# Performance work log

Hardware: AMD Instinct MI355X
Metric: run time of the kernel (lower is better)

The kernel has to match this reference:

```python
import jax, jax.numpy as jnp
import numpy as np
from jax import lax

NUM_HEADS = 8
HEAD_SIZE = 256  # hidden_size // num_heads

def _layernorm(x, g, b, eps=1e-5):
    mu = jnp.mean(x, axis=-1, keepdims=True)
    var = jnp.mean((x - mu) ** 2, axis=-1, keepdims=True)
    return (x - mu) * lax.rsqrt(var + eps) * g + b

def _groupnorm(x, g, b, num_groups, eps=1e-5):
    B, C = x.shape
    xr = x.reshape(B, num_groups, C // num_groups)
    mu = jnp.mean(xr, axis=-1, keepdims=True)
    var = jnp.mean((xr - mu) ** 2, axis=-1, keepdims=True)
    xn = ((xr - mu) * lax.rsqrt(var + eps)).reshape(B, C)
    return xn * g + b

def _block_diag(x, W, b):
    # x: (B, nb*fi), W: (nb, fi, fo), b: (nb, fo) -> (B, nb*fo)
    B = x.shape[0]
    nb, fi, fo = W.shape
    y = jnp.einsum('bnf,nfo->bno', x.reshape(B, nb, fi), W) + b
    return y.reshape(B, nb * fo)

def _causal_conv1d(x, w, b):
    # x: (B, L); w: (1,1,4). Pad-both-sides-3 then drop last 3 == left-pad 3.
    y = lax.conv_general_dilated(x[:, None, :], w, (1,), [(3, 0)])
    return y[:, 0, :] + b

def _mlstm_forward(x, ln_g, ln_b, Wupl, bupl, Wupr, bupr, conv_w, conv_b,
                   Wskip, bskip, Wq, bq, Wk, bk, Wv, bv, Wi, bi, Wf, bf,
                   Wo, bo, gn_g, gn_b, Wdown, bdown, c_prev, n_prev, m_prev):
    x_norm = _layernorm(x, ln_g, ln_b)
    x_up_left = x_norm @ Wupl + bupl           # (B, 2D)
    x_up_right = x_norm @ Wupr + bupr          # (B, H)
    x_conv = jax.nn.silu(_causal_conv1d(x_up_left, conv_w, conv_b))
    x_skip = x_conv @ Wskip + bskip            # (B, H)
    q = _block_diag(x_conv, Wq, bq)
    k = _block_diag(x_conv, Wk, bk) / (HEAD_SIZE ** 0.5)
    v = _block_diag(x_up_left, Wv, bv)
    i_tilde = x_conv @ Wi + bi
    f_tilde = x_conv @ Wf + bf
    o = jax.nn.sigmoid(x_up_left @ Wo + bo)
    m_t = jnp.maximum(f_tilde + m_prev, i_tilde)
    i_g = jnp.exp(i_tilde - m_t)
    f_g = jnp.exp(f_tilde + m_prev - m_t)
    c_t = f_g * c_prev + i_g * (v * k)
    n_t = f_g * n_prev + i_g * k
    denom = jnp.max(jnp.abs(n_t.T @ q), axis=1)  # (H,) broadcast over batch
    h_t = o * (c_t * q) / denom
    out = _groupnorm(h_t, gn_g, gn_b, NUM_HEADS) + x_skip
    out = out * jax.nn.silu(x_up_right)
    final = out @ Wdown + bdown + x
    return (final, h_t, c_t, n_t, m_t)

def setup_inputs():
    key = jax.random.key(0)
    ks = jax.random.split(key, 16)
    B, D, H, NB = 8192, 1024, 2048, 8
    UP = 2 * D
    rnd = lambda k, shp, s=0.02: jax.random.normal(k, shp, jnp.float32) * s
    return {
        'x': jax.random.normal(ks[0], (B, D), jnp.float32),
        'ln_g': jnp.ones((D,), jnp.float32), 'ln_b': jnp.zeros((D,), jnp.float32),
        'Wupl': rnd(ks[1], (D, UP)), 'bupl': jnp.zeros((UP,), jnp.float32),
        'Wupr': rnd(ks[2], (D, H)), 'bupr': jnp.zeros((H,), jnp.float32),
        'conv_w': rnd(ks[3], (1, 1, 4), 0.3), 'conv_b': jnp.zeros((1,), jnp.float32),
        'Wskip': rnd(ks[4], (UP, H)), 'bskip': jnp.zeros((H,), jnp.float32),
        'Wq': rnd(ks[5], (NB, UP // NB, H // NB)), 'bq': jnp.zeros((NB, H // NB), jnp.float32),
        'Wk': rnd(ks[6], (NB, UP // NB, H // NB)), 'bk': jnp.zeros((NB, H // NB), jnp.float32),
        'Wv': rnd(ks[7], (NB, UP // NB, H // NB)), 'bv': jnp.zeros((NB, H // NB), jnp.float32),
        'Wi': rnd(ks[8], (UP, H)), 'bi': jnp.zeros((H,), jnp.float32),
        'Wf': rnd(ks[9], (UP, H)), 'bf': jnp.zeros((H,), jnp.float32),
        'Wo': rnd(ks[10], (UP, H)), 'bo': jnp.zeros((H,), jnp.float32),
        'gn_g': jnp.ones((H,), jnp.float32), 'gn_b': jnp.zeros((H,), jnp.float32),
        'Wdown': rnd(ks[11], (H, D)), 'bdown': jnp.zeros((D,), jnp.float32),
        'c_prev': rnd(ks[12], (B, H)), 'n_prev': jnp.ones((B, H), jnp.float32),
        'm_prev': jnp.zeros((B, H), jnp.float32),
    }

def reference(x, ln_g, ln_b, Wupl, bupl, Wupr, bupr, conv_w, conv_b, Wskip, bskip,
              Wq, bq, Wk, bk, Wv, bv, Wi, bi, Wf, bf, Wo, bo, gn_g, gn_b,
              Wdown, bdown, c_prev, n_prev, m_prev):
    return _mlstm_forward(x, ln_g, ln_b, Wupl, bupl, Wupr, bupr, conv_w, conv_b,
                          Wskip, bskip, Wq, bq, Wk, bk, Wv, bv, Wi, bi, Wf, bf,
                          Wo, bo, gn_g, gn_b, Wdown, bdown, c_prev, n_prev, m_prev)
```

## Files before the change

### kernel.cpp

```cpp
#include <hip/hip_runtime.h>


typedef __bf16 bf16_t;
typedef bf16_t bf16x8 __attribute__((ext_vector_type(8)));
typedef bf16_t bf16x4 __attribute__((ext_vector_type(4)));
typedef float f32x4 __attribute__((ext_vector_type(4)));

#define B_ROWS 8192
#define DMODEL 1024
#define HDIM   2048

__device__ __forceinline__ void gload_lds16(const void* g, void* s) {
  __builtin_amdgcn_global_load_lds(
      (const __attribute__((address_space(1))) void*)g,
      (__attribute__((address_space(3))) void*)s, 16, 0, 0);
}

__device__ __forceinline__ float sigmoidf_(float x) { return 1.f / (1.f + __expf(-x)); }
__device__ __forceinline__ float siluf_(float x)    { return x / (1.f + __expf(-x)); }

__device__ __forceinline__ int xcd_swz(int lin, int nwg) {
  const int q = nwg >> 3, r = nwg & 7;
  const int xcd = lin & 7, sub = lin >> 3;
  return (xcd < r ? xcd * (q + 1) : r * (q + 1) + (xcd - r) * q) + sub;
}

__global__ __launch_bounds__(256) void wtrans_kernel(
    const float* __restrict__ in, bf16_t* __restrict__ out, int R, int C) {
  const int z = blockIdx.z;
  in  += (size_t)z * R * C;
  out += (size_t)z * R * C;
  __shared__ float tile[64][65];
  const int t = threadIdx.x;
  const int r0 = blockIdx.y * 64, c0 = blockIdx.x * 64;
#pragma unroll
  for (int j = 0; j < 4; ++j) {
    const int r = j * 16 + (t >> 4);
    const int c = (t & 15) * 4;
    float4 v = *(const float4*)&in[(size_t)(r0 + r) * C + c0 + c];
    tile[r][c] = v.x; tile[r][c + 1] = v.y; tile[r][c + 2] = v.z; tile[r][c + 3] = v.w;
  }
  __syncthreads();
#pragma unroll
  for (int j = 0; j < 2; ++j) {
    const int wi = j * 256 + t;
    const int oc = wi >> 3;
    const int orr = (wi & 7) * 8;
    bf16x8 v;
#pragma unroll
    for (int u = 0; u < 8; ++u) v[u] = (bf16_t)tile[orr + u][oc];
    *(bf16x8*)&out[(size_t)(c0 + oc) * R + r0 + orr] = v;
  }
}

__global__ __launch_bounds__(256) void ln_kernel(
    const float* __restrict__ x, const float* __restrict__ g,
    const float* __restrict__ b, bf16_t* __restrict__ out) {
  const int row = blockIdx.x;
  const int t = threadIdx.x;
  const float* xr = x + (size_t)row * DMODEL;
  float4 v = *(const float4*)&xr[t * 4];
  float s = v.x + v.y + v.z + v.w;
  float s2 = v.x * v.x + v.y * v.y + v.z * v.z + v.w * v.w;
#pragma unroll
  for (int off = 1; off < 64; off <<= 1) {
    s += __shfl_xor(s, off, 64);
    s2 += __shfl_xor(s2, off, 64);
  }
  __shared__ float ps[8];
  const int w = t >> 6;
  if ((t & 63) == 0) { ps[w] = s; ps[4 + w] = s2; }
  __syncthreads();
  s = ps[0] + ps[1] + ps[2] + ps[3];
  s2 = ps[4] + ps[5] + ps[6] + ps[7];
  const float mu = s / (float)DMODEL;
  const float var = s2 / (float)DMODEL - mu * mu;
  const float rstd = rsqrtf(var + 1e-5f);
  float4 gg = *(const float4*)&g[t * 4];
  float4 bb = *(const float4*)&b[t * 4];
  bf16x4 o;
  o[0] = (bf16_t)((v.x - mu) * rstd * gg.x + bb.x);
  o[1] = (bf16_t)((v.y - mu) * rstd * gg.y + bb.y);
  o[2] = (bf16_t)((v.z - mu) * rstd * gg.z + bb.z);
  o[3] = (bf16_t)((v.w - mu) * rstd * gg.w + bb.w);
  *(bf16x4*)&out[(size_t)row * DMODEL + t * 4] = o;
}

__global__ __launch_bounds__(256) void conv_kernel(
    const bf16_t* __restrict__ xin, const float* __restrict__ cw,
    const float* __restrict__ cb, bf16_t* __restrict__ yb) {
  const size_t idx = (size_t)blockIdx.x * blockDim.x + threadIdx.x;
  const int row = (int)(idx >> 9);
  const int c0 = ((int)idx & 511) * 4;
  const bf16_t* xr = xin + (size_t)row * HDIM;
  const float w0 = cw[0], w1 = cw[1], w2 = cw[2], w3 = cw[3], bb = cb[0];
  float xm3 = 0.f, xm2 = 0.f, xm1 = 0.f;
  if (c0 > 0) {
    bf16x4 p = *(const bf16x4*)&xr[c0 - 4];
    xm3 = (float)p[1]; xm2 = (float)p[2]; xm1 = (float)p[3];
  }
  bf16x4 xv4 = *(const bf16x4*)&xr[c0];
  float x0 = (float)xv4[0], x1 = (float)xv4[1], x2 = (float)xv4[2], x3 = (float)xv4[3];
  float y0 = w0 * xm3 + w1 * xm2 + w2 * xm1 + w3 * x0 + bb;
  float y1 = w0 * xm2 + w1 * xm1 + w2 * x0 + w3 * x1 + bb;
  float y2 = w0 * xm1 + w1 * x0 + w2 * x1 + w3 * x2 + bb;
  float y3 = w0 * x0 + w1 * x1 + w2 * x2 + w3 * x3 + bb;
  bf16x4 yb4;
  yb4[0] = (bf16_t)siluf_(y0); yb4[1] = (bf16_t)siluf_(y1);
  yb4[2] = (bf16_t)siluf_(y2); yb4[3] = (bf16_t)siluf_(y3);
  *(bf16x4*)&yb[(size_t)row * HDIM + c0] = yb4;
}

__global__ __launch_bounds__(256) void hgn_kernel(
    const bf16_t* __restrict__ o_pre, const float* __restrict__ q,
    const float* __restrict__ c_t, const float* __restrict__ denomf,
    const bf16_t* __restrict__ skip, const bf16_t* __restrict__ upr,
    const float* __restrict__ gn_g, const float* __restrict__ gn_b,
    float* __restrict__ h_out, bf16_t* __restrict__ act_out) {
  const int row = blockIdx.x;
  const int t = threadIdx.x;
  const size_t base = (size_t)row * HDIM + t * 8;
  const int i0 = t * 8;
  bf16x8 o8 = *(const bf16x8*)&o_pre[base];
  float h[8];
  float s = 0.f, s2 = 0.f;
#pragma unroll
  for (int j = 0; j < 2; ++j) {
    float4 qv = *(const float4*)&q[base + j * 4];
    float4 cv = *(const float4*)&c_t[base + j * 4];
#pragma unroll
    for (int u = 0; u < 4; ++u) {
      const int k = j * 4 + u;
      float hv = sigmoidf_((float)o8[k]) * ((const float*)&cv)[u] *
                 ((const float*)&qv)[u] / denomf[i0 + k];
      h[k] = hv;
      s += hv;
      s2 += hv * hv;
    }
  }
#pragma unroll
  for (int off = 1; off < 32; off <<= 1) {
    s += __shfl_xor(s, off, 64);
    s2 += __shfl_xor(s2, off, 64);
  }
  const float mu = s / 256.f;
  const float var = s2 / 256.f - mu * mu;
  const float rstd = rsqrtf(var + 1e-5f);
  float4 h0 = {h[0], h[1], h[2], h[3]};
  float4 h1 = {h[4], h[5], h[6], h[7]};
  *(float4*)&h_out[base] = h0;
  *(float4*)&h_out[base + 4] = h1;
  bf16x8 sk8 = *(const bf16x8*)&skip[base];
  bf16x8 up8 = *(const bf16x8*)&upr[base];
  bf16x8 a8;
#pragma unroll
  for (int j = 0; j < 2; ++j) {
    float4 gv = *(const float4*)&gn_g[i0 + j * 4];
    float4 bv = *(const float4*)&gn_b[i0 + j * 4];
#pragma unroll
    for (int u = 0; u < 4; ++u) {
      const int k = j * 4 + u;
      float y = (h[k] - mu) * rstd * ((const float*)&gv)[u] + ((const float*)&bv)[u];
      y = (y + (float)sk8[k]) * siluf_((float)up8[k]);
      a8[k] = (bf16_t)y;
    }
  }
  *(bf16x8*)&act_out[base] = a8;
}

template <int OUTMODE, bool RES>
__global__ __launch_bounds__(256) void gemm_kernel(
    const bf16_t* __restrict__ A, int lda, const bf16_t* __restrict__ Bt, int ldb,
    const float* __restrict__ bias, float* __restrict__ C, bf16_t* __restrict__ Cb,
    int ldc, const float* __restrict__ res, int ldres, int K, float scale,
    int zA, long long zB, int zBias, int zC) {
  const int z = blockIdx.z;
  A += (size_t)z * zA;
  Bt += (size_t)z * zB;
  if (bias) bias += (size_t)z * zBias;
  if (OUTMODE == 0) C += (size_t)z * zC; else Cb += (size_t)z * zC;
  const int brow = blockIdx.y * 128;
  const int bcol = blockIdx.x * 128;
  __shared__ bf16_t As[128 * 32];
  __shared__ bf16_t Bs[128 * 32];
  const int tid = threadIdx.x;
  const int w = tid >> 6, l = tid & 63;
  const int wr = w >> 1, wc = w & 1;
  const int lr = l & 15, kg = l >> 4;
  const int l4 = l & 3, ld4 = l >> 2;

  f32x4 acc[4][4];
  const f32x4 fzero = {0.f, 0.f, 0.f, 0.f};
#pragma unroll
  for (int m = 0; m < 4; ++m)
#pragma unroll
    for (int n = 0; n < 4; ++n) acc[m][n] = fzero;

  for (int kt = 0; kt < K; kt += 32) {
#pragma unroll
    for (int j = 0; j < 2; ++j) {
      const int rowX = w * 32 + j * 16 + ld4;
      gload_lds16(A + (size_t)(brow + rowX) * lda + kt + l4 * 8, &As[w * 1024 + j * 512]);
      gload_lds16(Bt + (size_t)(bcol + rowX) * ldb + kt + l4 * 8, &Bs[w * 1024 + j * 512]);
    }
    __syncthreads();
    bf16x8 a[4], b[4];
#pragma unroll
    for (int m = 0; m < 4; ++m)
      a[m] = *(const bf16x8*)&As[(wr * 64 + m * 16 + lr) * 32 + kg * 8];
#pragma unroll
    for (int n = 0; n < 4; ++n)
      b[n] = *(const bf16x8*)&Bs[(wc * 64 + n * 16 + lr) * 32 + kg * 8];
#pragma unroll
    for (int m = 0; m < 4; ++m)
#pragma unroll
      for (int n = 0; n < 4; ++n)
        acc[m][n] = __builtin_amdgcn_mfma_f32_16x16x32_bf16(a[m], b[n], acc[m][n], 0, 0, 0);
    __syncthreads();
  }

#pragma unroll
  for (int m = 0; m < 4; ++m) {
    const int row0 = brow + wr * 64 + m * 16 + kg * 4;
#pragma unroll
    for (int n = 0; n < 4; ++n) {
      const int col = bcol + wc * 64 + n * 16 + lr;
      const float bv = bias ? bias[col] : 0.f;
#pragma unroll
      for (int r = 0; r < 4; ++r) {
        const int row = row0 + r;
        float v = (acc[m][n][r] + bv) * scale;
        if (RES) v += res[(size_t)row * ldres + col];
        if (OUTMODE == 0) C[(size_t)row * ldc + col] = v;
        else Cb[(size_t)row * ldc + col] = (bf16_t)v;
      }
    }
  }
}

template <int OUTMODE , bool RES>
__global__ __launch_bounds__(512, 2) void gemm256_kernel(
    const bf16_t* __restrict__ A, int lda, const bf16_t* __restrict__ Bt, int ldb,
    const float* __restrict__ bias, float* __restrict__ C, bf16_t* __restrict__ Cb,
    int ldc, const float* __restrict__ res, int ldres, int K, float scale,
    long long zA, long long zB, long long zC) {
  const int z = blockIdx.z;
  A += (size_t)z * zA;
  Bt += (size_t)z * zB;
  if (OUTMODE == 0) C += (size_t)z * zC; else Cb += (size_t)z * zC;

  const int nwg = gridDim.x * gridDim.y;
  const int lin2 = xcd_swz(blockIdx.y * gridDim.x + blockIdx.x, nwg);
  const int bx = lin2 % gridDim.x, by = lin2 / gridDim.x;
  const int brow = by * 256, bcol = bx * 256;

  __shared__ bf16_t As[2][256 * 64];
  __shared__ bf16_t Bs[2][256 * 64];

  const int tid = threadIdx.x;
  const int l = tid & 63;
  const int w = tid >> 6;
  const int wr = w >> 2, wn = w & 3;
  const int lr = l & 15, kg = l >> 4;
  const int srow = tid >> 3;
  const int sslot = (tid & 7) ^ (srow & 7);

  f32x4 acc[8][4];
  const f32x4 fzero = {0.f, 0.f, 0.f, 0.f};
#pragma unroll
  for (int m = 0; m < 8; ++m)
#pragma unroll
    for (int n = 0; n < 4; ++n) acc[m][n] = fzero;

  const int NT = K >> 6;
  const bf16_t* Ag = A + (size_t)brow * lda;
  const bf16_t* Bg = Bt + (size_t)bcol * ldb;

  auto stage = [&](int t, int buf) {
    const size_t kof = (size_t)t * 64 + sslot * 8;
#pragma unroll
    for (int j = 0; j < 4; ++j) {
      const int r = j * 64 + srow;
      gload_lds16(Ag + (size_t)r * lda + kof, (char*)&As[buf][0] + (j * 512 + tid) * 16);
      gload_lds16(Bg + (size_t)r * ldb + kof, (char*)&Bs[buf][0] + (j * 512 + tid) * 16);
    }
  };

  stage(0, 0);
  stage(1, 1);

  for (int t = 0; t < NT; ++t) {
    if (t < NT - 1) asm volatile("s_waitcnt vmcnt(8)" ::: "memory");
    else            asm volatile("s_waitcnt vmcnt(0)" ::: "memory");
    __builtin_amdgcn_s_barrier();
    const int buf = t & 1;
#pragma unroll
    for (int kk = 0; kk < 2; ++kk) {
      bf16x8 a[8], b[4];
#pragma unroll
      for (int n = 0; n < 4; ++n) {
        const int r = wn * 64 + n * 16 + lr;
        b[n] = *(const bf16x8*)&Bs[buf][r * 64 + (((kk * 4 + kg) ^ (r & 7)) * 8)];
      }
#pragma unroll
      for (int m = 0; m < 8; ++m) {
        const int r = wr * 128 + m * 16 + lr;
        a[m] = *(const bf16x8*)&As[buf][r * 64 + (((kk * 4 + kg) ^ (r & 7)) * 8)];
      }
      __builtin_amdgcn_s_setprio(1);
#pragma unroll
      for (int m = 0; m < 8; ++m)
#pragma unroll
        for (int n = 0; n < 4; ++n)
          acc[m][n] = __builtin_amdgcn_mfma_f32_16x16x32_bf16(a[m], b[n], acc[m][n], 0, 0, 0);
      __builtin_amdgcn_s_setprio(0);
    }
    asm volatile("s_waitcnt lgkmcnt(0)" ::: "memory");
    __builtin_amdgcn_sched_barrier(0);
    __builtin_amdgcn_s_barrier();
    if (t + 2 < NT) stage(t + 2, buf);
  }

#pragma unroll
  for (int m = 0; m < 8; ++m) {
    const int row0 = brow + wr * 128 + m * 16 + kg * 4;
#pragma unroll
    for (int n = 0; n < 4; ++n) {
      const int col = bcol + wn * 64 + n * 16 + lr;
      const float bvv = bias ? bias[col] : 0.f;
#pragma unroll
      for (int r = 0; r < 4; ++r) {
        const int row = row0 + r;
        float v = (acc[m][n][r] + bvv) * scale;
        if (RES) v += res[(size_t)row * ldres + col];
        if (OUTMODE == 0) C[(size_t)row * ldc + col] = v;
        else Cb[(size_t)row * ldc + col] = (bf16_t)v;
      }
    }
  }
}

__global__ __launch_bounds__(512, 2) void ifgate256_kernel(
    const bf16_t* __restrict__ A,
    const bf16_t* __restrict__ Bi, const bf16_t* __restrict__ Bf,
    const float* __restrict__ bi, const float* __restrict__ bfv,
    const float* __restrict__ m_prev, const float* __restrict__ c_prev,
    const float* __restrict__ n_prev,
    const bf16_t* __restrict__ vb, const bf16_t* __restrict__ kb,
    float* __restrict__ m_out, float* __restrict__ c_out, float* __restrict__ n_out) {
  const int nwg = gridDim.x * gridDim.y;
  const int lin2 = xcd_swz(blockIdx.y * gridDim.x + blockIdx.x, nwg);
  const int bx = lin2 % gridDim.x, by = lin2 / gridDim.x;
  const int brow = by * 256, bcol = bx * 128;

  __shared__ bf16_t As[2][256 * 64];
  __shared__ bf16_t Bis[2][128 * 64];
  __shared__ bf16_t Bfs[2][128 * 64];

  const int tid = threadIdx.x;
  const int l = tid & 63;
  const int w = tid >> 6;
  const int wr = w >> 2, wn = w & 3;
  const int lr = l & 15, kg = l >> 4;
  const int srow = tid >> 3;
  const int sslot = (tid & 7) ^ (srow & 7);

  f32x4 acci[8][2], accf[8][2];
  const f32x4 fzero = {0.f, 0.f, 0.f, 0.f};
#pragma unroll
  for (int m = 0; m < 8; ++m)
#pragma unroll
    for (int n = 0; n < 2; ++n) { acci[m][n] = fzero; accf[m][n] = fzero; }

  const int NT = HDIM >> 6;
  const bf16_t* Ag = A + (size_t)brow * HDIM;
  const bf16_t* Big = Bi + (size_t)bcol * HDIM;
  const bf16_t* Bfg = Bf + (size_t)bcol * HDIM;

  auto stage = [&](int t, int buf) {
    const size_t kof = (size_t)t * 64 + sslot * 8;
#pragma unroll
    for (int j = 0; j < 4; ++j) {
      const int r = j * 64 + srow;
      gload_lds16(Ag + (size_t)r * HDIM + kof, (char*)&As[buf][0] + (j * 512 + tid) * 16);
    }
#pragma unroll
    for (int j = 0; j < 2; ++j) {
      const int r = j * 64 + srow;
      gload_lds16(Big + (size_t)r * HDIM + kof, (char*)&Bis[buf][0] + (j * 512 + tid) * 16);
      gload_lds16(Bfg + (size_t)r * HDIM + kof, (char*)&Bfs[buf][0] + (j * 512 + tid) * 16);
    }
  };

  stage(0, 0);
  stage(1, 1);

  for (int t = 0; t < NT; ++t) {
    if (t < NT - 1) asm volatile("s_waitcnt vmcnt(8)" ::: "memory");
    else            asm volatile("s_waitcnt vmcnt(0)" ::: "memory");
    __builtin_amdgcn_s_barrier();
    const int buf = t & 1;
#pragma unroll
    for (int kk = 0; kk < 2; ++kk) {
      bf16x8 a[8], b1[2], b2[2];
#pragma unroll
      for (int n = 0; n < 2; ++n) {
        const int r = wn * 32 + n * 16 + lr;
        const int eo = r * 64 + (((kk * 4 + kg) ^ (r & 7)) * 8);
        b1[n] = *(const bf16x8*)&Bis[buf][eo];
        b2[n] = *(const bf16x8*)&Bfs[buf][eo];
      }
#pragma unroll
      for (int m = 0; m < 8; ++m) {
        const int r = wr * 128 + m * 16 + lr;
        a[m] = *(const bf16x8*)&As[buf][r * 64 + (((kk * 4 + kg) ^ (r & 7)) * 8)];
      }
      __builtin_amdgcn_s_setprio(1);
#pragma unroll
      for (int m = 0; m < 8; ++m)
#pragma unroll
        for (int n = 0; n < 2; ++n) {
          acci[m][n] = __builtin_amdgcn_mfma_f32_16x16x32_bf16(a[m], b1[n], acci[m][n], 0, 0, 0);
          accf[m][n] = __builtin_amdgcn_mfma_f32_16x16x32_bf16(a[m], b2[n], accf[m][n], 0, 0, 0);
        }
      __builtin_amdgcn_s_setprio(0);
    }
    asm volatile("s_waitcnt lgkmcnt(0)" ::: "memory");
    __builtin_amdgcn_sched_barrier(0);
    __builtin_amdgcn_s_barrier();
    if (t + 2 < NT) stage(t + 2, buf);
  }

#pragma unroll
  for (int m = 0; m < 8; ++m) {
    const int row0 = brow + wr * 128 + m * 16 + kg * 4;
#pragma unroll
    for (int n = 0; n < 2; ++n) {
      const int col = bcol + wn * 32 + n * 16 + lr;
      const float biv = bi[col], bfvv = bfv[col];
#pragma unroll
      for (int r = 0; r < 4; ++r) {
        const int row = row0 + r;
        const size_t idx = (size_t)row * HDIM + col;
        const float it = acci[m][n][r] + biv;
        const float ft = accf[m][n][r] + bfvv;
        const float m1 = m_prev[idx];
        const float mt = fmaxf(ft + m1, it);
        const float ig = __expf(it - mt);
        const float fg = __expf(ft + m1 - mt);
        const float v1 = (float)vb[idx], k1 = (float)kb[idx];
        m_out[idx] = mt;
        c_out[idx] = fg * c_prev[idx] + ig * (v1 * k1);
        n_out[idx] = fg * n_prev[idx] + ig * k1;
      }
    }
  }
}

__global__ __launch_bounds__(256) void denom_reduce_kernel(
    const float* __restrict__ part, float* __restrict__ dmaxf) {
  const int i = blockIdx.x;
  const int t = threadIdx.x;
  float vmax = 0.f;
#pragma unroll
  for (int u = 0; u < 8; ++u) {
    const int j = u * 256 + t;
    float s = 0.f;
#pragma unroll
    for (int zz = 0; zz < 4; ++zz)
      s += part[(size_t)zz * HDIM * HDIM + (size_t)i * HDIM + j];
    vmax = fmaxf(vmax, fabsf(s));
  }
#pragma unroll
  for (int off = 1; off < 64; off <<= 1) vmax = fmaxf(vmax, __shfl_xor(vmax, off, 64));
  __shared__ float ps[4];
  if ((t & 63) == 0) ps[t >> 6] = vmax;
  __syncthreads();
  if (t == 0) dmaxf[i] = fmaxf(fmaxf(ps[0], ps[1]), fmaxf(ps[2], ps[3]));
}

extern "C" void kernel_launch(void* const* d_in, const int* in_sizes, int n_in,
                              void* d_out, int out_size, void* d_ws, size_t ws_size,
                              hipStream_t stream) {
  (void)in_sizes; (void)n_in; (void)out_size; (void)ws_size;
  const float* x      = (const float*)d_in[0];
  const float* ln_g   = (const float*)d_in[1];
  const float* ln_b   = (const float*)d_in[2];
  const float* Wupl   = (const float*)d_in[3];
  const float* bupl   = (const float*)d_in[4];
  const float* Wupr   = (const float*)d_in[5];
  const float* bupr   = (const float*)d_in[6];
  const float* conv_w = (const float*)d_in[7];
  const float* conv_b = (const float*)d_in[8];
  const float* Wskip  = (const float*)d_in[9];
  const float* bskip  = (const float*)d_in[10];
  const float* Wq     = (const float*)d_in[11];
  const float* bq     = (const float*)d_in[12];
  const float* Wk     = (const float*)d_in[13];
  const float* bk     = (const float*)d_in[14];
  const float* Wv     = (const float*)d_in[15];
  const float* bv     = (const float*)d_in[16];
  const float* Wi     = (const float*)d_in[17];
  const float* bi     = (const float*)d_in[18];
  const float* Wf     = (const float*)d_in[19];
  const float* bf_    = (const float*)d_in[20];
  const float* Wo     = (const float*)d_in[21];
  const float* bo     = (const float*)d_in[22];
  const float* gn_g   = (const float*)d_in[23];
  const float* gn_b   = (const float*)d_in[24];
  const float* Wdown  = (const float*)d_in[25];
  const float* bdown  = (const float*)d_in[26];
  const float* c_prev = (const float*)d_in[27];
  const float* n_prev = (const float*)d_in[28];
  const float* m_prev = (const float*)d_in[29];

  float* out_final = (float*)d_out;
  float* out_h = out_final + (size_t)B_ROWS * DMODEL;
  float* out_c = out_h + (size_t)B_ROWS * HDIM;
  float* out_n = out_c + (size_t)B_ROWS * HDIM;
  float* out_m = out_n + (size_t)B_ROWS * HDIM;

  char* ws = (char*)d_ws;
  size_t off = 0;
  auto alloc = [&](size_t bytes) -> void* {
    off = (off + 255) & ~(size_t)255;
    void* p = ws + off;
    off += bytes;
    return p;
  };
  const size_t BH = (size_t)B_ROWS * HDIM;
  const size_t BD = (size_t)B_ROWS * DMODEL;

  bf16_t* WuplT = (bf16_t*)alloc((size_t)DMODEL * HDIM * 2);
  bf16_t* WuprT = (bf16_t*)alloc((size_t)DMODEL * HDIM * 2);
  bf16_t* WskipT = (bf16_t*)alloc((size_t)HDIM * HDIM * 2);
  bf16_t* WiT = (bf16_t*)alloc((size_t)HDIM * HDIM * 2);
  bf16_t* WfT = (bf16_t*)alloc((size_t)HDIM * HDIM * 2);
  bf16_t* WoT = (bf16_t*)alloc((size_t)HDIM * HDIM * 2);
  bf16_t* WdownT = (bf16_t*)alloc((size_t)HDIM * DMODEL * 2);
  bf16_t* WqT = (bf16_t*)alloc((size_t)8 * 256 * 256 * 2);
  bf16_t* WkT = (bf16_t*)alloc((size_t)8 * 256 * 256 * 2);
  bf16_t* WvT = (bf16_t*)alloc((size_t)8 * 256 * 256 * 2);
  bf16_t* xnorm_b = (bf16_t*)alloc(BD * 2);
  bf16_t* xupl_b = (bf16_t*)alloc(BH * 2);
  bf16_t* xupr_b = (bf16_t*)alloc(BH * 2);
  bf16_t* xconv_b = (bf16_t*)alloc(BH * 2);
  bf16_t* xskip_b = (bf16_t*)alloc(BH * 2);
  bf16_t* o_b = (bf16_t*)alloc(BH * 2);
  float*  q_f = (float*)alloc(BH * 4);
  bf16_t* k_b = (bf16_t*)alloc(BH * 2);
  bf16_t* v_b = (bf16_t*)alloc(BH * 2);
  bf16_t* qT_b = (bf16_t*)alloc(BH * 2);
  bf16_t* nT_b = (bf16_t*)alloc(BH * 2);
  bf16_t* act_b = (bf16_t*)alloc(BH * 2);
  float*  part = (float*)alloc((size_t)4 * HDIM * HDIM * 4);
  float*  dmaxf = (float*)alloc(HDIM * 4);

  wtrans_kernel<<<dim3(HDIM / 64, DMODEL / 64, 1), 256, 0, stream>>>(Wupl, WuplT, DMODEL, HDIM);
  wtrans_kernel<<<dim3(HDIM / 64, DMODEL / 64, 1), 256, 0, stream>>>(Wupr, WuprT, DMODEL, HDIM);
  wtrans_kernel<<<dim3(HDIM / 64, HDIM / 64, 1), 256, 0, stream>>>(Wskip, WskipT, HDIM, HDIM);
  wtrans_kernel<<<dim3(HDIM / 64, HDIM / 64, 1), 256, 0, stream>>>(Wi, WiT, HDIM, HDIM);
  wtrans_kernel<<<dim3(HDIM / 64, HDIM / 64, 1), 256, 0, stream>>>(Wf, WfT, HDIM, HDIM);
  wtrans_kernel<<<dim3(HDIM / 64, HDIM / 64, 1), 256, 0, stream>>>(Wo, WoT, HDIM, HDIM);
  wtrans_kernel<<<dim3(DMODEL / 64, HDIM / 64, 1), 256, 0, stream>>>(Wdown, WdownT, HDIM, DMODEL);
  wtrans_kernel<<<dim3(4, 4, 8), 256, 0, stream>>>(Wq, WqT, 256, 256);
  wtrans_kernel<<<dim3(4, 4, 8), 256, 0, stream>>>(Wk, WkT, 256, 256);
  wtrans_kernel<<<dim3(4, 4, 8), 256, 0, stream>>>(Wv, WvT, 256, 256);

  ln_kernel<<<B_ROWS, 256, 0, stream>>>(x, ln_g, ln_b, xnorm_b);

  gemm256_kernel<2, false><<<dim3(HDIM / 256, B_ROWS / 256, 1), 512, 0, stream>>>(
      xnorm_b, DMODEL, WuplT, DMODEL, bupl, nullptr, xupl_b, HDIM, nullptr, 0,
      DMODEL, 1.f, 0, 0, 0);
  gemm256_kernel<2, false><<<dim3(HDIM / 256, B_ROWS / 256, 1), 512, 0, stream>>>(
      xnorm_b, DMODEL, WuprT, DMODEL, bupr, nullptr, xupr_b, HDIM, nullptr, 0,
      DMODEL, 1.f, 0, 0, 0);

  conv_kernel<<<(unsigned)(BH / 4 / 256), 256, 0, stream>>>(xupl_b, conv_w, conv_b, xconv_b);

  gemm256_kernel<2, false><<<dim3(HDIM / 256, B_ROWS / 256, 1), 512, 0, stream>>>(
      xconv_b, HDIM, WskipT, HDIM, bskip, nullptr, xskip_b, HDIM, nullptr, 0,
      HDIM, 1.f, 0, 0, 0);
  gemm256_kernel<2, false><<<dim3(HDIM / 256, B_ROWS / 256, 1), 512, 0, stream>>>(
      xupl_b, HDIM, WoT, HDIM, bo, nullptr, o_b, HDIM, nullptr, 0,
      HDIM, 1.f, 0, 0, 0);

  gemm_kernel<0, false><<<dim3(2, B_ROWS / 128, 8), 256, 0, stream>>>(
      xconv_b, HDIM, WqT, 256, bq, q_f, nullptr, HDIM, nullptr, 0,
      256, 1.f, 256, 256 * 256, 256, 256);
  gemm_kernel<2, false><<<dim3(2, B_ROWS / 128, 8), 256, 0, stream>>>(
      xconv_b, HDIM, WkT, 256, bk, nullptr, k_b, HDIM, nullptr, 0,
      256, 0.0625f, 256, 256 * 256, 256, 256);
  gemm_kernel<2, false><<<dim3(2, B_ROWS / 128, 8), 256, 0, stream>>>(
      xupl_b, HDIM, WvT, 256, bv, nullptr, v_b, HDIM, nullptr, 0,
      256, 1.f, 256, 256 * 256, 256, 256);

  ifgate256_kernel<<<dim3(HDIM / 128, B_ROWS / 256, 1), 512, 0, stream>>>(
      xconv_b, WiT, WfT, bi, bf_, m_prev, c_prev, n_prev, v_b, k_b,
      out_m, out_c, out_n);

  wtrans_kernel<<<dim3(HDIM / 64, B_ROWS / 64, 1), 256, 0, stream>>>(q_f, qT_b, B_ROWS, HDIM);
  wtrans_kernel<<<dim3(HDIM / 64, B_ROWS / 64, 1), 256, 0, stream>>>(out_n, nT_b, B_ROWS, HDIM);

  gemm256_kernel<0, false><<<dim3(HDIM / 256, HDIM / 256, 4), 512, 0, stream>>>(
      nT_b, B_ROWS, qT_b, B_ROWS, nullptr, part, nullptr, HDIM, nullptr, 0,
      2048, 1.f, 2048, 2048, (long long)HDIM * HDIM);
  denom_reduce_kernel<<<HDIM, 256, 0, stream>>>(part, dmaxf);

  hgn_kernel<<<B_ROWS, 256, 0, stream>>>(o_b, q_f, out_c, dmaxf, xskip_b,
                                         xupr_b, gn_g, gn_b, out_h, act_b);

  gemm256_kernel<0, true><<<dim3(DMODEL / 256, B_ROWS / 256, 1), 512, 0, stream>>>(
      act_b, HDIM, WdownT, HDIM, bdown, out_final, nullptr, DMODEL, x, DMODEL,
      HDIM, 1.f, 0, 0, 0);
}
```

Measured before the change: 1.351 ms.

## Split GEMM K-tiles into half-stages with finer-grained prefetch; store q in bf16

The main GEMM kernels now split each 64-wide K tile into two 32-wide halves with a new swizzle. Loads for the next tile are issued in between MFMA groups, with per-half waitcnt and barrier, so global-to-LDS traffic overlaps compute more finely and the trailing lgkmcnt wait and barrier go away. The q projection is stored as bf16 instead of fp32, which halves its write and read traffic and needs a new bf16 transpose kernel. The down projection uses a new 256x128-tile GEMM to put more workgroups on the N=1024 output. Risks are extra barriers per tile and slightly lower precision for q in h_t.

```diff
diff --git a/kernel.cpp b/kernel.cpp
--- a/kernel.cpp
+++ b/kernel.cpp
@@ -39,6 +39,32 @@
     const int c = (t & 15) * 4;
     float4 v = *(const float4*)&in[(size_t)(r0 + r) * C + c0 + c];
     tile[r][c] = v.x; tile[r][c + 1] = v.y; tile[r][c + 2] = v.z; tile[r][c + 3] = v.w;
+  }
+  __syncthreads();
+#pragma unroll
+  for (int j = 0; j < 2; ++j) {
+    const int wi = j * 256 + t;
+    const int oc = wi >> 3;
+    const int orr = (wi & 7) * 8;
+    bf16x8 v;
+#pragma unroll
+    for (int u = 0; u < 8; ++u) v[u] = (bf16_t)tile[orr + u][oc];
+    *(bf16x8*)&out[(size_t)(c0 + oc) * R + r0 + orr] = v;
+  }
+}
+
+__global__ __launch_bounds__(256) void wtransb_kernel(
+    const bf16_t* __restrict__ in, bf16_t* __restrict__ out, int R, int C) {
+  __shared__ float tile[64][65];
+  const int t = threadIdx.x;
+  const int r0 = blockIdx.y * 64, c0 = blockIdx.x * 64;
+#pragma unroll
+  for (int j = 0; j < 4; ++j) {
+    const int r = j * 16 + (t >> 4);
+    const int c = (t & 15) * 4;
+    bf16x4 v = *(const bf16x4*)&in[(size_t)(r0 + r) * C + c0 + c];
+    tile[r][c] = (float)v[0]; tile[r][c + 1] = (float)v[1];
+    tile[r][c + 2] = (float)v[2]; tile[r][c + 3] = (float)v[3];
   }
   __syncthreads();
 #pragma unroll
@@ -112,7 +138,7 @@
 }
 
 __global__ __launch_bounds__(256) void hgn_kernel(
-    const bf16_t* __restrict__ o_pre, const float* __restrict__ q,
+    const bf16_t* __restrict__ o_pre, const bf16_t* __restrict__ q,
     const float* __restrict__ c_t, const float* __restrict__ denomf,
     const bf16_t* __restrict__ skip, const bf16_t* __restrict__ upr,
     const float* __restrict__ gn_g, const float* __restrict__ gn_b,
@@ -122,17 +148,17 @@
   const size_t base = (size_t)row * HDIM + t * 8;
   const int i0 = t * 8;
   bf16x8 o8 = *(const bf16x8*)&o_pre[base];
+  bf16x8 q8 = *(const bf16x8*)&q[base];
   float h[8];
   float s = 0.f, s2 = 0.f;
 #pragma unroll
   for (int j = 0; j < 2; ++j) {
-    float4 qv = *(const float4*)&q[base + j * 4];
     float4 cv = *(const float4*)&c_t[base + j * 4];
 #pragma unroll
     for (int u = 0; u < 4; ++u) {
       const int k = j * 4 + u;
       float hv = sigmoidf_((float)o8[k]) * ((const float*)&cv)[u] *
-                 ((const float*)&qv)[u] / denomf[i0 + k];
+                 (float)q8[k] / denomf[i0 + k];
       h[k] = hv;
       s += hv;
       s2 += hv * hv;
@@ -238,6 +264,8 @@
   }
 }
 
+#define SWZ_RD(r, kg) (((kg) ^ (((r) >> 1) & 3)) * 8)
+
 template <int OUTMODE , bool RES>
 __global__ __launch_bounds__(512, 2) void gemm256_kernel(
     const bf16_t* __restrict__ A, int lda, const bf16_t* __restrict__ Bt, int ldb,
@@ -254,16 +282,14 @@
   const int bx = lin2 % gridDim.x, by = lin2 / gridDim.x;
   const int brow = by * 256, bcol = bx * 256;
 
-  __shared__ bf16_t As[2][256 * 64];
-  __shared__ bf16_t Bs[2][256 * 64];
+  __shared__ bf16_t As[2][2][256 * 32];
+  __shared__ bf16_t Bs[2][2][256 * 32];
 
   const int tid = threadIdx.x;
   const int l = tid & 63;
   const int w = tid >> 6;
   const int wr = w >> 2, wn = w & 3;
   const int lr = l & 15, kg = l >> 4;
-  const int srow = tid >> 3;
-  const int sslot = (tid & 7) ^ (srow & 7);
 
   f32x4 acc[8][4];
   const f32x4 fzero = {0.f, 0.f, 0.f, 0.f};
@@ -276,49 +302,103 @@
   const bf16_t* Ag = A + (size_t)brow * lda;
   const bf16_t* Bg = Bt + (size_t)bcol * ldb;
 
-  auto stage = [&](int t, int buf) {
-    const size_t kof = (size_t)t * 64 + sslot * 8;
-#pragma unroll
-    for (int j = 0; j < 4; ++j) {
-      const int r = j * 64 + srow;
-      gload_lds16(Ag + (size_t)r * lda + kof, (char*)&As[buf][0] + (j * 512 + tid) * 16);
-      gload_lds16(Bg + (size_t)r * ldb + kof, (char*)&Bs[buf][0] + (j * 512 + tid) * 16);
+  auto stageA = [&](int d, int kh, int kbase) {
+#pragma unroll
+    for (int j = 0; j < 2; ++j) {
+      const int L = j * 512 + tid;
+      const int row = L >> 2;
+      const int s = (L & 3) ^ ((L >> 3) & 3);
+      gload_lds16(Ag + (size_t)row * lda + kbase + kh * 32 + s * 8,
+                  (char*)&As[d][kh][0] + L * 16);
     }
   };
-
-  stage(0, 0);
-  stage(1, 1);
+  auto stageB = [&](int d, int kh, int kbase) {
+#pragma unroll
+    for (int j = 0; j < 2; ++j) {
+      const int L = j * 512 + tid;
+      const int row = L >> 2;
+      const int s = (L & 3) ^ ((L >> 3) & 3);
+      gload_lds16(Bg + (size_t)row * ldb + kbase + kh * 32 + s * 8,
+                  (char*)&Bs[d][kh][0] + L * 16);
+    }
+  };
+
+  stageA(0, 0, 0); stageB(0, 0, 0); stageA(0, 1, 0); stageB(0, 1, 0);
 
   for (int t = 0; t < NT; ++t) {
-    if (t < NT - 1) asm volatile("s_waitcnt vmcnt(8)" ::: "memory");
-    else            asm volatile("s_waitcnt vmcnt(0)" ::: "memory");
+    const int d = t & 1;
+    const int kn = (t + 1) * 64;
+    const bool st = (t + 1 < NT);
+    bf16x8 a[4], b[4];
+
+    asm volatile("s_waitcnt vmcnt(4)" ::: "memory");
     __builtin_amdgcn_s_barrier();
-    const int buf = t & 1;
-#pragma unroll
-    for (int kk = 0; kk < 2; ++kk) {
-      bf16x8 a[8], b[4];
-#pragma unroll
-      for (int n = 0; n < 4; ++n) {
-        const int r = wn * 64 + n * 16 + lr;
-        b[n] = *(const bf16x8*)&Bs[buf][r * 64 + (((kk * 4 + kg) ^ (r & 7)) * 8)];
-      }
-#pragma unroll
-      for (int m = 0; m < 8; ++m) {
-        const int r = wr * 128 + m * 16 + lr;
-        a[m] = *(const bf16x8*)&As[buf][r * 64 + (((kk * 4 + kg) ^ (r & 7)) * 8)];
-      }
-      __builtin_amdgcn_s_setprio(1);
-#pragma unroll
-      for (int m = 0; m < 8; ++m)
-#pragma unroll
-        for (int n = 0; n < 4; ++n)
-          acc[m][n] = __builtin_amdgcn_mfma_f32_16x16x32_bf16(a[m], b[n], acc[m][n], 0, 0, 0);
-      __builtin_amdgcn_s_setprio(0);
-    }
-    asm volatile("s_waitcnt lgkmcnt(0)" ::: "memory");
-    __builtin_amdgcn_sched_barrier(0);
+    if (st) stageA(d ^ 1, 0, kn);
+#pragma unroll
+    for (int n = 0; n < 4; ++n) {
+      const int r = wn * 64 + n * 16 + lr;
+      b[n] = *(const bf16x8*)&Bs[d][0][r * 32 + SWZ_RD(r, kg)];
+    }
+#pragma unroll
+    for (int mm = 0; mm < 4; ++mm) {
+      const int r = wr * 128 + mm * 16 + lr;
+      a[mm] = *(const bf16x8*)&As[d][0][r * 32 + SWZ_RD(r, kg)];
+    }
+    __builtin_amdgcn_s_setprio(1);
+#pragma unroll
+    for (int mm = 0; mm < 4; ++mm)
+#pragma unroll
+      for (int n = 0; n < 4; ++n)
+        acc[mm][n] = __builtin_amdgcn_mfma_f32_16x16x32_bf16(a[mm], b[n], acc[mm][n], 0, 0, 0);
+    __builtin_amdgcn_s_setprio(0);
+    if (st) stageB(d ^ 1, 0, kn);
+#pragma unroll
+    for (int mm = 0; mm < 4; ++mm) {
+      const int r = wr * 128 + (4 + mm) * 16 + lr;
+      a[mm] = *(const bf16x8*)&As[d][0][r * 32 + SWZ_RD(r, kg)];
+    }
+    __builtin_amdgcn_s_setprio(1);
+#pragma unroll
+    for (int mm = 0; mm < 4; ++mm)
+#pragma unroll
+      for (int n = 0; n < 4; ++n)
+        acc[4 + mm][n] = __builtin_amdgcn_mfma_f32_16x16x32_bf16(a[mm], b[n], acc[4 + mm][n], 0, 0, 0);
+    __builtin_amdgcn_s_setprio(0);
+
+    if (t == NT - 1) asm volatile("s_waitcnt vmcnt(0)" ::: "memory");
+    else             asm volatile("s_waitcnt vmcnt(4)" ::: "memory");
     __builtin_amdgcn_s_barrier();
-    if (t + 2 < NT) stage(t + 2, buf);
+    if (st) stageA(d ^ 1, 1, kn);
+#pragma unroll
+    for (int n = 0; n < 4; ++n) {
+      const int r = wn * 64 + n * 16 + lr;
+      b[n] = *(const bf16x8*)&Bs[d][1][r * 32 + SWZ_RD(r, kg)];
+    }
+#pragma unroll
+    for (int mm = 0; mm < 4; ++mm) {
+      const int r = wr * 128 + mm * 16 + lr;
+      a[mm] = *(const bf16x8*)&As[d][1][r * 32 + SWZ_RD(r, kg)];
+    }
+    __builtin_amdgcn_s_setprio(1);
+#pragma unroll
+    for (int mm = 0; mm < 4; ++mm)
+#pragma unroll
+      for (int n = 0; n < 4; ++n)
+        acc[mm][n] = __builtin_amdgcn_mfma_f32_16x16x32_bf16(a[mm], b[n], acc[mm][n], 0, 0, 0);
+    __builtin_amdgcn_s_setprio(0);
+    if (st) stageB(d ^ 1, 1, kn);
+#pragma unroll
+    for (int mm = 0; mm < 4; ++mm) {
+      const int r = wr * 128 + (4 + mm) * 16 + lr;
+      a[mm] = *(const bf16x8*)&As[d][1][r * 32 + SWZ_RD(r, kg)];
+    }
+    __builtin_amdgcn_s_setprio(1);
+#pragma unroll
+    for (int mm = 0; mm < 4; ++mm)
+#pragma unroll
+      for (int n = 0; n < 4; ++n)
+        acc[4 + mm][n] = __builtin_amdgcn_mfma_f32_16x16x32_bf16(a[mm], b[n], acc[4 + mm][n], 0, 0, 0);
+    __builtin_amdgcn_s_setprio(0);
   }
 
 #pragma unroll
@@ -327,6 +407,120 @@
 #pragma unroll
     for (int n = 0; n < 4; ++n) {
       const int col = bcol + wn * 64 + n * 16 + lr;
+      const float bvv = bias ? bias[col] : 0.f;
+#pragma unroll
+      for (int r = 0; r < 4; ++r) {
+        const int row = row0 + r;
+        float v = (acc[m][n][r] + bvv) * scale;
+        if (RES) v += res[(size_t)row * ldres + col];
+        if (OUTMODE == 0) C[(size_t)row * ldc + col] = v;
+        else Cb[(size_t)row * ldc + col] = (bf16_t)v;
+      }
+    }
+  }
+}
+
+template <int OUTMODE, bool RES>
+__global__ __launch_bounds__(512, 2) void gemm256n128_kernel(
+    const bf16_t* __restrict__ A, int lda, const bf16_t* __restrict__ Bt, int ldb,
+    const float* __restrict__ bias, float* __restrict__ C, bf16_t* __restrict__ Cb,
+    int ldc, const float* __restrict__ res, int ldres, int K, float scale) {
+  const int nwg = gridDim.x * gridDim.y;
+  const int lin2 = xcd_swz(blockIdx.y * gridDim.x + blockIdx.x, nwg);
+  const int bx = lin2 % gridDim.x, by = lin2 / gridDim.x;
+  const int brow = by * 256, bcol = bx * 128;
+
+  __shared__ bf16_t As[2][2][256 * 32];
+  __shared__ bf16_t Bs[2][2][128 * 32];
+
+  const int tid = threadIdx.x;
+  const int l = tid & 63;
+  const int w = tid >> 6;
+  const int wr = w >> 2, wn = w & 3;
+  const int lr = l & 15, kg = l >> 4;
+
+  f32x4 acc[8][2];
+  const f32x4 fzero = {0.f, 0.f, 0.f, 0.f};
+#pragma unroll
+  for (int m = 0; m < 8; ++m)
+#pragma unroll
+    for (int n = 0; n < 2; ++n) acc[m][n] = fzero;
+
+  const int NT = K >> 6;
+  const bf16_t* Ag = A + (size_t)brow * lda;
+  const bf16_t* Bg = Bt + (size_t)bcol * ldb;
+
+  auto stageA = [&](int d, int kh, int kbase) {
+#pragma unroll
+    for (int j = 0; j < 2; ++j) {
+      const int L = j * 512 + tid;
+      const int row = L >> 2;
+      const int s = (L & 3) ^ ((L >> 3) & 3);
+      gload_lds16(Ag + (size_t)row * lda + kbase + kh * 32 + s * 8,
+                  (char*)&As[d][kh][0] + L * 16);
+    }
+  };
+  auto stageB = [&](int d, int kh, int kbase) {
+    const int L = tid;
+    const int row = L >> 2;
+    const int s = (L & 3) ^ ((L >> 3) & 3);
+    gload_lds16(Bg + (size_t)row * ldb + kbase + kh * 32 + s * 8,
+                (char*)&Bs[d][kh][0] + L * 16);
+  };
+
+  stageA(0, 0, 0); stageB(0, 0, 0); stageA(0, 1, 0); stageB(0, 1, 0);
+
+  for (int t = 0; t < NT; ++t) {
+    const int d = t & 1;
+    const int kn = (t + 1) * 64;
+    const bool st = (t + 1 < NT);
+    bf16x8 a[4], b[2];
+
+#pragma unroll
+    for (int kk = 0; kk < 2; ++kk) {
+      if (kk == 0 || t < NT - 1) asm volatile("s_waitcnt vmcnt(3)" ::: "memory");
+      else                       asm volatile("s_waitcnt vmcnt(0)" ::: "memory");
+      __builtin_amdgcn_s_barrier();
+      if (st) stageA(d ^ 1, kk, kn);
+#pragma unroll
+      for (int n = 0; n < 2; ++n) {
+        const int r = wn * 32 + n * 16 + lr;
+        b[n] = *(const bf16x8*)&Bs[d][kk][r * 32 + SWZ_RD(r, kg)];
+      }
+#pragma unroll
+      for (int mm = 0; mm < 4; ++mm) {
+        const int r = wr * 128 + mm * 16 + lr;
+        a[mm] = *(const bf16x8*)&As[d][kk][r * 32 + SWZ_RD(r, kg)];
+      }
+      __builtin_amdgcn_s_setprio(1);
+#pragma unroll
+      for (int mm = 0; mm < 4; ++mm)
+#pragma unroll
+        for (int n = 0; n < 2; ++n)
+          acc[mm][n] = __builtin_amdgcn_mfma_f32_16x16x32_bf16(a[mm], b[n], acc[mm][n], 0, 0, 0);
+      __builtin_amdgcn_s_setprio(0);
+      if (st) stageB(d ^ 1, kk, kn);
+#pragma unroll
+      for (int mm = 0; mm < 4; ++mm) {
+        const int r = wr * 128 + (4 + mm) * 16 + lr;
+        a[mm] = *(const bf16x8*)&As[d][kk][r * 32 + SWZ_RD(r, kg)];
+      }
+      __builtin_amdgcn_s_setprio(1);
+#pragma unroll
+      for (int mm = 0; mm < 4; ++mm)
+#pragma unroll
+        for (int n = 0; n < 2; ++n)
+          acc[4 + mm][n] = __builtin_amdgcn_mfma_f32_16x16x32_bf16(a[mm], b[n], acc[4 + mm][n], 0, 0, 0);
+      __builtin_amdgcn_s_setprio(0);
+    }
+  }
+
+#pragma unroll
+  for (int m = 0; m < 8; ++m) {
+    const int row0 = brow + wr * 128 + m * 16 + kg * 4;
+#pragma unroll
+    for (int n = 0; n < 2; ++n) {
+      const int col = bcol + wn * 32 + n * 16 + lr;
       const float bvv = bias ? bias[col] : 0.f;
 #pragma unroll
       for (int r = 0; r < 4; ++r) {
@@ -353,17 +547,15 @@
   const int bx = lin2 % gridDim.x, by = lin2 / gridDim.x;
   const int brow = by * 256, bcol = bx * 128;
 
-  __shared__ bf16_t As[2][256 * 64];
-  __shared__ bf16_t Bis[2][128 * 64];
-  __shared__ bf16_t Bfs[2][128 * 64];
+  __shared__ bf16_t As[2][2][256 * 32];
+  __shared__ bf16_t Bis[2][2][128 * 32];
+  __shared__ bf16_t Bfs[2][2][128 * 32];
 
   const int tid = threadIdx.x;
   const int l = tid & 63;
   const int w = tid >> 6;
   const int wr = w >> 2, wn = w & 3;
   const int lr = l & 15, kg = l >> 4;
-  const int srow = tid >> 3;
-  const int sslot = (tid & 7) ^ (srow & 7);
 
   f32x4 acci[8][2], accf[8][2];
   const f32x4 fzero = {0.f, 0.f, 0.f, 0.f};
@@ -377,58 +569,77 @@
   const bf16_t* Big = Bi + (size_t)bcol * HDIM;
   const bf16_t* Bfg = Bf + (size_t)bcol * HDIM;
 
-  auto stage = [&](int t, int buf) {
-    const size_t kof = (size_t)t * 64 + sslot * 8;
-#pragma unroll
-    for (int j = 0; j < 4; ++j) {
-      const int r = j * 64 + srow;
-      gload_lds16(Ag + (size_t)r * HDIM + kof, (char*)&As[buf][0] + (j * 512 + tid) * 16);
-    }
+  auto stageA = [&](int d, int kh, int kbase) {
 #pragma unroll
     for (int j = 0; j < 2; ++j) {
-      const int r = j * 64 + srow;
-      gload_lds16(Big + (size_t)r * HDIM + kof, (char*)&Bis[buf][0] + (j * 512 + tid) * 16);
-      gload_lds16(Bfg + (size_t)r * HDIM + kof, (char*)&Bfs[buf][0] + (j * 512 + tid) * 16);
+      const int L = j * 512 + tid;
+      const int row = L >> 2;
+      const int s = (L & 3) ^ ((L >> 3) & 3);
+      gload_lds16(Ag + (size_t)row * HDIM + kbase + kh * 32 + s * 8,
+                  (char*)&As[d][kh][0] + L * 16);
     }
   };
-
-  stage(0, 0);
-  stage(1, 1);
+  auto stageBB = [&](int d, int kh, int kbase) {
+    const int L = tid;
+    const int row = L >> 2;
+    const int s = (L & 3) ^ ((L >> 3) & 3);
+    gload_lds16(Big + (size_t)row * HDIM + kbase + kh * 32 + s * 8,
+                (char*)&Bis[d][kh][0] + L * 16);
+    gload_lds16(Bfg + (size_t)row * HDIM + kbase + kh * 32 + s * 8,
+                (char*)&Bfs[d][kh][0] + L * 16);
+  };
+
+  stageA(0, 0, 0); stageBB(0, 0, 0); stageA(0, 1, 0); stageBB(0, 1, 0);
 
   for (int t = 0; t < NT; ++t) {
-    if (t < NT - 1) asm volatile("s_waitcnt vmcnt(8)" ::: "memory");
-    else            asm volatile("s_waitcnt vmcnt(0)" ::: "memory");
-    __builtin_amdgcn_s_barrier();
-    const int buf = t & 1;
+    const int d = t & 1;
+    const int kn = (t + 1) * 64;
+    const bool st = (t + 1 < NT);
+    bf16x8 a[4], b1[2], b2[2];
+
 #pragma unroll
     for (int kk = 0; kk < 2; ++kk) {
-      bf16x8 a[8], b1[2], b2[2];
+      if (kk == 0 || t < NT - 1) asm volatile("s_waitcnt vmcnt(4)" ::: "memory");
+      else                       asm volatile("s_waitcnt vmcnt(0)" ::: "memory");
+      __builtin_amdgcn_s_barrier();
+      if (st) stageA(d ^ 1, kk, kn);
 #pragma unroll
       for (int n = 0; n < 2; ++n) {
         const int r = wn * 32 + n * 16 + lr;
-        const int eo = r * 64 + (((kk * 4 + kg) ^ (r & 7)) * 8);
-        b1[n] = *(const bf16x8*)&Bis[buf][eo];
-        b2[n] = *(const bf16x8*)&Bfs[buf][eo];
-      }
-#pragma unroll
-      for (int m = 0; m < 8; ++m) {
-        const int r = wr * 128 + m * 16 + lr;
-        a[m] = *(const bf16x8*)&As[buf][r * 64 + (((kk * 4 + kg) ^ (r & 7)) * 8)];
+        const int eo = r * 32 + SWZ_RD(r, kg);
+        b1[n] = *(const bf16x8*)&Bis[d][kk][eo];
+        b2[n] = *(const bf16x8*)&Bfs[d][kk][eo];
+      }
+#pragma unroll
+      for (int mm = 0; mm < 4; ++mm) {
+        const int r = wr * 128 + mm * 16 + lr;
+        a[mm] = *(const bf16x8*)&As[d][kk][r * 32 + SWZ_RD(r, kg)];
       }
       __builtin_amdgcn_s_setprio(1);
 #pragma unroll
-      for (int m = 0; m < 8; ++m)
+      for (int mm = 0; mm < 4; ++mm)
 #pragma unroll
         for (int n = 0; n < 2; ++n) {
-          acci[m][n] = __builtin_amdgcn_mfma_f32_16x16x32_bf16(a[m], b1[n], acci[m][n], 0, 0, 0);
-          accf[m][n] = __builtin_amdgcn_mfma_f32_16x16x32_bf16(a[m], b2[n], accf[m][n], 0, 0, 0);
+          acci[mm][n] = __builtin_amdgcn_mfma_f32_16x16x32_bf16(a[mm], b1[n], acci[mm][n], 0, 0, 0);
+          accf[mm][n] = __builtin_amdgcn_mfma_f32_16x16x32_bf16(a[mm], b2[n], accf[mm][n], 0, 0, 0);
         }
       __builtin_amdgcn_s_setprio(0);
-    }
-    asm volatile("s_waitcnt lgkmcnt(0)" ::: "memory");
-    __builtin_amdgcn_sched_barrier(0);
-    __builtin_amdgcn_s_barrier();
-    if (t + 2 < NT) stage(t + 2, buf);
+      if (st) stageBB(d ^ 1, kk, kn);
+#pragma unroll
+      for (int mm = 0; mm < 4; ++mm) {
+        const int r = wr * 128 + (4 + mm) * 16 + lr;
+        a[mm] = *(const bf16x8*)&As[d][kk][r * 32 + SWZ_RD(r, kg)];
+      }
+      __builtin_amdgcn_s_setprio(1);
+#pragma unroll
+      for (int mm = 0; mm < 4; ++mm)
+#pragma unroll
+        for (int n = 0; n < 2; ++n) {
+          acci[4 + mm][n] = __builtin_amdgcn_mfma_f32_16x16x32_bf16(a[mm], b1[n], acci[4 + mm][n], 0, 0, 0);
+          accf[4 + mm][n] = __builtin_amdgcn_mfma_f32_16x16x32_bf16(a[mm], b2[n], accf[4 + mm][n], 0, 0, 0);
+        }
+      __builtin_amdgcn_s_setprio(0);
+    }
   }
 
 #pragma unroll
@@ -547,7 +758,7 @@
   bf16_t* xconv_b = (bf16_t*)alloc(BH * 2);
   bf16_t* xskip_b = (bf16_t*)alloc(BH * 2);
   bf16_t* o_b = (bf16_t*)alloc(BH * 2);
-  float*  q_f = (float*)alloc(BH * 4);
+  bf16_t* q_b = (bf16_t*)alloc(BH * 2);
   bf16_t* k_b = (bf16_t*)alloc(BH * 2);
   bf16_t* v_b = (bf16_t*)alloc(BH * 2);
   bf16_t* qT_b = (bf16_t*)alloc(BH * 2);
@@ -585,8 +796,8 @@
       xupl_b, HDIM, WoT, HDIM, bo, nullptr, o_b, HDIM, nullptr, 0,
       HDIM, 1.f, 0, 0, 0);
 
-  gemm_kernel<0, false><<<dim3(2, B_ROWS / 128, 8), 256, 0, stream>>>(
-      xconv_b, HDIM, WqT, 256, bq, q_f, nullptr, HDIM, nullptr, 0,
+  gemm_kernel<2, false><<<dim3(2, B_ROWS / 128, 8), 256, 0, stream>>>(
+      xconv_b, HDIM, WqT, 256, bq, nullptr, q_b, HDIM, nullptr, 0,
       256, 1.f, 256, 256 * 256, 256, 256);
   gemm_kernel<2, false><<<dim3(2, B_ROWS / 128, 8), 256, 0, stream>>>(
       xconv_b, HDIM, WkT, 256, bk, nullptr, k_b, HDIM, nullptr, 0,
@@ -599,7 +810,7 @@
       xconv_b, WiT, WfT, bi, bf_, m_prev, c_prev, n_prev, v_b, k_b,
       out_m, out_c, out_n);
 
-  wtrans_kernel<<<dim3(HDIM / 64, B_ROWS / 64, 1), 256, 0, stream>>>(q_f, qT_b, B_ROWS, HDIM);
+  wtransb_kernel<<<dim3(HDIM / 64, B_ROWS / 64, 1), 256, 0, stream>>>(q_b, qT_b, B_ROWS, HDIM);
   wtrans_kernel<<<dim3(HDIM / 64, B_ROWS / 64, 1), 256, 0, stream>>>(out_n, nT_b, B_ROWS, HDIM);
 
   gemm256_kernel<0, false><<<dim3(HDIM / 256, HDIM / 256, 4), 512, 0, stream>>>(
@@ -607,10 +818,10 @@
       2048, 1.f, 2048, 2048, (long long)HDIM * HDIM);
   denom_reduce_kernel<<<HDIM, 256, 0, stream>>>(part, dmaxf);
 
-  hgn_kernel<<<B_ROWS, 256, 0, stream>>>(o_b, q_f, out_c, dmaxf, xskip_b,
+  hgn_kernel<<<B_ROWS, 256, 0, stream>>>(o_b, q_b, out_c, dmaxf, xskip_b,
                                          xupr_b, gn_g, gn_b, out_h, act_b);
 
-  gemm256_kernel<0, true><<<dim3(DMODEL / 256, B_ROWS / 256, 1), 512, 0, stream>>>(
+  gemm256n128_kernel<0, true><<<dim3(DMODEL / 128, B_ROWS / 256, 1), 512, 0, stream>>>(
       act_b, HDIM, WdownT, HDIM, bdown, out_final, nullptr, DMODEL, x, DMODEL,
-      HDIM, 1.f, 0, 0, 0);
-}
+      HDIM, 1.f);
+}
```

After: 1.346 ms. About the same (-0.4%).
